# Kernel tuning notes

Hardware: AMD Instinct MI355X
Metric: run time of the kernel (lower is better)

The kernel has to match this reference:

```python
import jax, jax.numpy as jnp
import numpy as np

N = 100000   # nodes
E = 1250000  # edges
D = 64       # in = hidden = out channels
LN_EPS = 1e-5
L2_EPS = 1e-12


def setup_inputs() -> dict:
    key = jax.random.key(0)
    ks = jax.random.split(key, 16)
    s = 1.0 / np.sqrt(D)
    inp = {
        "x": jax.random.normal(ks[0], (N, D), jnp.float32),
        "edge_index": jax.random.randint(ks[1], (2, E), 0, N, dtype=jnp.int64),
    }
    for i in range(3):  # SAGEConv i: out = mean_aggr @ Wl + bl + x @ Wr
        inp[f"Wl{i}"] = jax.random.normal(ks[2 + 2 * i], (D, D), jnp.float32) * s
        inp[f"bl{i}"] = jnp.zeros((D,), jnp.float32)
        inp[f"Wr{i}"] = jax.random.normal(ks[3 + 2 * i], (D, D), jnp.float32) * s
    for i in range(2):  # LayerNorm after layers 0,1
        inp[f"g{i}"] = jnp.ones((D,), jnp.float32)
        inp[f"b{i}"] = jnp.zeros((D,), jnp.float32)
    return inp


def _sage_conv(x, src, dst, Wl, bl, Wr):
    # PyG SAGEConv(aggr='mean'): lin_l(mean of neighbor msgs) + lin_r(x)
    agg = jax.ops.segment_sum(x[src], dst, num_segments=N)          # [N, D]
    deg = jax.ops.segment_sum(jnp.ones((src.shape[0],), x.dtype), dst, num_segments=N)
    mean = agg / jnp.maximum(deg, 1.0)[:, None]
    return mean @ Wl + bl + x @ Wr


def _layer_norm(h, g, b):
    mu = jnp.mean(h, axis=-1, keepdims=True)
    var = jnp.mean((h - mu) ** 2, axis=-1, keepdims=True)
    return (h - mu) * jax.lax.rsqrt(var + LN_EPS) * g + b


def reference(x, edge_index, Wl0, bl0, Wr0, Wl1, bl1, Wr1, Wl2, bl2, Wr2, g0, b0, g1, b1):
    src, dst = edge_index[0], edge_index[1]
    Ws = [(Wl0, bl0, Wr0), (Wl1, bl1, Wr1), (Wl2, bl2, Wr2)]
    lns = [(g0, b0), (g1, b1)]
    h = x
    for i in range(3):
        res = h  # residual projections are Identity (equal dims)
        h = _sage_conv(h, src, dst, *Ws[i])
        if i < 2:
            h = _layer_norm(h, *lns[i])
            h = jax.nn.relu(h)
            h = h + res
            # dropout is identity in eval mode
        else:
            h = h + res
    # F.normalize(p=2, dim=1)
    nrm = jnp.sqrt(jnp.sum(h * h, axis=1, keepdims=True))
    return h / jnp.maximum(nrm, L2_EPS)
```

## Files before the change

kernel.cpp:

```cpp
#include <hip/hip_runtime.h>

#define DD   64
#define WSTR 136
#define SSTR 72
#define BSH  9
#define BNODES 512
#define BCAPSH 13

typedef unsigned int uint32;
typedef __attribute__((ext_vector_type(8))) short short8;
typedef __attribute__((ext_vector_type(4))) float f32x4;

__device__ __forceinline__ unsigned short f2bf_rne(float f) {
    uint32 u = __float_as_uint(f);
    u += 0x7fffu + ((u >> 16) & 1u);
    return (unsigned short)(u >> 16);
}
__device__ __forceinline__ float bf_lo(uint32 w) { return __uint_as_float(w << 16); }
__device__ __forceinline__ float bf_hi(uint32 w) { return __uint_as_float(w & 0xffff0000u); }
__device__ __forceinline__ float bf2f(unsigned short s) {
    return __uint_as_float(((uint32)s) << 16);
}

__global__ __launch_bounds__(256) void cvt_kernel(const float* __restrict__ x,
                                                  unsigned short* __restrict__ xb,
                                                  int n4, int* __restrict__ gCnt) {
    if (blockIdx.x == 0 && threadIdx.x < 256) gCnt[threadIdx.x] = 0;
    int i = blockIdx.x * 256 + threadIdx.x;
    if (i < n4) {
        float4 v = ((const float4*)x)[i];
        ushort4 p;
        p.x = f2bf_rne(v.x); p.y = f2bf_rne(v.y);
        p.z = f2bf_rne(v.z); p.w = f2bf_rne(v.w);
        ((ushort4*)xb)[i] = p;
    }
}

__global__ __launch_bounds__(1024) void bucket_kernel(const int* __restrict__ src,
                                                      const int* __restrict__ dst,
                                                      int* __restrict__ gCnt,
                                                      int2* __restrict__ buf, int E) {
    __shared__ int ldsCnt[256];
    __shared__ int base[256];
    const int t = threadIdx.x;
    if (t < 256) ldsCnt[t] = 0;
    __syncthreads();

    const int e0 = blockIdx.x * 4096;
    int bk[4], rk[4], sv[4], dv[4];
#pragma unroll
    for (int k = 0; k < 4; ++k) {
        int e = e0 + k * 1024 + t;
        bk[k] = -1;
        if (e < E) {
            dv[k] = dst[e];
            sv[k] = src[e];
            bk[k] = dv[k] >> BSH;
            rk[k] = atomicAdd(&ldsCnt[bk[k]], 1);
        }
    }
    __syncthreads();
    if (t < 256 && ldsCnt[t] > 0) base[t] = atomicAdd(&gCnt[t], ldsCnt[t]);
    __syncthreads();
#pragma unroll
    for (int k = 0; k < 4; ++k) {
        if (bk[k] >= 0) {
            int pos = (bk[k] << BCAPSH) + base[bk[k]] + rk[k];
            buf[pos] = make_int2(sv[k], dv[k]);
        }
    }
}

__global__ __launch_bounds__(512) void csr_build(const int2* __restrict__ buf,
                                                 const int* __restrict__ gCnt,
                                                 int* __restrict__ offsets,
                                                 int* __restrict__ csr, int N, int E) {
    __shared__ int c1[BNODES];
    __shared__ int s[BNODES];
    __shared__ int sg2[256];
    const int b = blockIdx.x;
    const int t = threadIdx.x;
    if (t < 256) sg2[t] = gCnt[t];
    c1[t] = 0;
    __syncthreads();
    for (int d = 1; d < 256; d <<= 1) {
        int v = (t < 256 && t >= d) ? sg2[t - d] : 0;
        __syncthreads();
        if (t < 256 && t >= d) sg2[t] += v;
        __syncthreads();
    }
    const int base = (b == 0) ? 0 : sg2[b - 1];
    const int cnt = gCnt[b];
    const int2* bb = buf + ((size_t)b << BCAPSH);
    for (int i = t; i < cnt; i += 512) atomicAdd(&c1[bb[i].y & (BNODES - 1)], 1);
    __syncthreads();

    int v = c1[t];
    s[t] = v;
    __syncthreads();
    for (int d = 1; d < BNODES; d <<= 1) {
        int u = (t >= d) ? s[t - d] : 0;
        __syncthreads();
        if (t >= d) s[t] += u;
        __syncthreads();
    }
    int excl = s[t] - v;
    const int node = (b << BSH) + t;
    if (node < N) offsets[node] = base + excl;
    if (b == 0 && t == 0) offsets[N] = E;
    __syncthreads();
    s[t] = excl;
    c1[t] = 0;
    __syncthreads();

    for (int i = t; i < cnt; i += 512) {
        int2 e = bb[i];
        int d = e.y & (BNODES - 1);
        int r = atomicAdd(&c1[d], 1);
        csr[base + s[d] + r] = e.x;
    }
}

template <int MODE>
__global__ __launch_bounds__(256, 4) void sage_layer(
    const unsigned short* __restrict__ hbin,
    const int* __restrict__ offsets,
    const int* __restrict__ csr,
    const float* __restrict__ Wl,
    const float* __restrict__ bl,
    const float* __restrict__ Wr,
    const float* __restrict__ g,
    const float* __restrict__ bta,
    unsigned short* __restrict__ hbout,
    float* __restrict__ out,
    int N) {
    __shared__ unsigned short sWt[64 * WSTR];
    __shared__ unsigned short sSelf[64 * SSTR];
    __shared__ unsigned short sMean[64 * SSTR];
    __shared__ float sbl[DD], sg[DD], sb[DD];

    const int t = threadIdx.x;
    const int nbase = blockIdx.x * 64;

    for (int idx = t; idx < 2 * DD * DD; idx += 256) {
        int k = idx >> 6, c = idx & 63;
        float v = (k < DD) ? Wl[idx] : Wr[idx - DD * DD];
        sWt[c * WSTR + k] = f2bf_rne(v);
    }
    if (t < DD) {
        sbl[t] = bl[t];
        if (MODE == 0) { sg[t] = g[t]; sb[t] = bta[t]; }
    }

#pragma unroll
    for (int r = 0; r < 2; ++r) {
        int idx = r * 256 + t;
        int row = idx >> 3;
        int qq  = idx & 7;
        int n   = min(nbase + row, N - 1);
        uint4 v = ((const uint4*)(hbin + (size_t)n * DD))[qq];
        *(uint4*)(&sSelf[row * SSTR + qq * 8]) = v;
    }

    {
        const int grp = t >> 3;
        const int q   = t & 7;
#pragma unroll 1
        for (int rep = 0; rep < 2; ++rep) {
            int local = grp + rep * 32;
            int node  = nbase + local;
            float a0 = 0.f, a1 = 0.f, a2 = 0.f, a3 = 0.f,
                  a4 = 0.f, a5 = 0.f, a6 = 0.f, a7 = 0.f;
            int deg = 0;
            if (node < N) {
                int off0 = offsets[node];
                int off1 = offsets[node + 1];
                deg = off1 - off0;
                for (int j = off0; j < off1; j += 8) {
                    uint4 v[8];
#pragma unroll
                    for (int s = 0; s < 8; ++s) {
                        uint4 tt = make_uint4(0u, 0u, 0u, 0u);
                        int idx = j + s;
                        if (idx < off1) {
                            int sn = __builtin_nontemporal_load(&csr[idx]);
                            tt = ((const uint4*)(hbin + (size_t)sn * DD))[q];
                        }
                        v[s] = tt;
                    }
#pragma unroll
                    for (int s = 0; s < 8; ++s) {
                        a0 += bf_lo(v[s].x); a1 += bf_hi(v[s].x);
                        a2 += bf_lo(v[s].y); a3 += bf_hi(v[s].y);
                        a4 += bf_lo(v[s].z); a5 += bf_hi(v[s].z);
                        a6 += bf_lo(v[s].w); a7 += bf_hi(v[s].w);
                    }
                }
            }
            float invd = 1.0f / fmaxf((float)deg, 1.0f);
            ushort4 pa, pb;
            pa.x = f2bf_rne(a0 * invd); pa.y = f2bf_rne(a1 * invd);
            pa.z = f2bf_rne(a2 * invd); pa.w = f2bf_rne(a3 * invd);
            pb.x = f2bf_rne(a4 * invd); pb.y = f2bf_rne(a5 * invd);
            pb.z = f2bf_rne(a6 * invd); pb.w = f2bf_rne(a7 * invd);
            *(ushort4*)(&sMean[local * SSTR + q * 8])     = pa;
            *(ushort4*)(&sMean[local * SSTR + q * 8 + 4]) = pb;
        }
    }
    __syncthreads();

    const int wave = t >> 6;
    const int lane = t & 63;
    const int quad = lane >> 4;
    const int n16  = lane & 15;
    const int lbase = wave * 16;

    short8 af[4];
    af[0] = *(const short8*)(&sMean[(lbase + n16) * SSTR + quad * 8]);
    af[1] = *(const short8*)(&sMean[(lbase + n16) * SSTR + 32 + quad * 8]);
    af[2] = *(const short8*)(&sSelf[(lbase + n16) * SSTR + quad * 8]);
    af[3] = *(const short8*)(&sSelf[(lbase + n16) * SSTR + 32 + quad * 8]);

    f32x4 acc[4];
#pragma unroll
    for (int j = 0; j < 4; ++j) {
        float bv = sbl[j * 16 + n16];
        acc[j] = (f32x4){bv, bv, bv, bv};
    }
#pragma unroll
    for (int s = 0; s < 4; ++s) {
#pragma unroll
        for (int j = 0; j < 4; ++j) {
            short8 bf = *(const short8*)(&sWt[(j * 16 + n16) * WSTR + s * 32 + quad * 8]);
            acc[j] = __builtin_amdgcn_mfma_f32_16x16x32_bf16(af[s], bf, acc[j], 0, 0, 0);
        }
    }

#pragma unroll
    for (int i = 0; i < 4; ++i) {
        const int lrow = lbase + quad * 4 + i;
        const int rr   = nbase + lrow;
        float res[4];
#pragma unroll
        for (int j = 0; j < 4; ++j)
            res[j] = bf2f(sSelf[lrow * SSTR + j * 16 + n16]);
        float o[4];
        if (MODE == 0) {
            float s4 = acc[0][i] + acc[1][i] + acc[2][i] + acc[3][i];
            s4 += __shfl_xor(s4, 1, 64);
            s4 += __shfl_xor(s4, 2, 64);
            s4 += __shfl_xor(s4, 4, 64);
            s4 += __shfl_xor(s4, 8, 64);
            float mu = s4 * (1.0f / 64.0f);
            float d0 = acc[0][i] - mu, d1 = acc[1][i] - mu,
                  d2 = acc[2][i] - mu, d3 = acc[3][i] - mu;
            float qq = d0 * d0 + d1 * d1 + d2 * d2 + d3 * d3;
            qq += __shfl_xor(qq, 1, 64);
            qq += __shfl_xor(qq, 2, 64);
            qq += __shfl_xor(qq, 4, 64);
            qq += __shfl_xor(qq, 8, 64);
            float rstd = rsqrtf(qq * (1.0f / 64.0f) + 1e-5f);
            o[0] = fmaxf(d0 * rstd * sg[ 0 + n16] + sb[ 0 + n16], 0.f) + res[0];
            o[1] = fmaxf(d1 * rstd * sg[16 + n16] + sb[16 + n16], 0.f) + res[1];
            o[2] = fmaxf(d2 * rstd * sg[32 + n16] + sb[32 + n16], 0.f) + res[2];
            o[3] = fmaxf(d3 * rstd * sg[48 + n16] + sb[48 + n16], 0.f) + res[3];
        } else {
            o[0] = acc[0][i] + res[0];
            o[1] = acc[1][i] + res[1];
            o[2] = acc[2][i] + res[2];
            o[3] = acc[3][i] + res[3];
            float qq = o[0] * o[0] + o[1] * o[1] + o[2] * o[2] + o[3] * o[3];
            qq += __shfl_xor(qq, 1, 64);
            qq += __shfl_xor(qq, 2, 64);
            qq += __shfl_xor(qq, 4, 64);
            qq += __shfl_xor(qq, 8, 64);
            float inv = 1.0f / fmaxf(sqrtf(qq), 1e-12f);
            o[0] *= inv; o[1] *= inv; o[2] *= inv; o[3] *= inv;
        }
        if (rr < N) {
#pragma unroll
            for (int j = 0; j < 4; ++j) {
                if (MODE == 0)
                    hbout[(size_t)rr * DD + j * 16 + n16] = f2bf_rne(o[j]);
                else
                    out[(size_t)rr * DD + j * 16 + n16] = o[j];
            }
        }
    }
}

extern "C" void kernel_launch(void* const* d_in, const int* in_sizes, int n_in,
                              void* d_out, int out_size, void* d_ws, size_t ws_size,
                              hipStream_t stream) {
    const float* x   = (const float*)d_in[0];
    const int*   ei  = (const int*)d_in[1];
    const float* Wl0 = (const float*)d_in[2];
    const float* bl0 = (const float*)d_in[3];
    const float* Wr0 = (const float*)d_in[4];
    const float* Wl1 = (const float*)d_in[5];
    const float* bl1 = (const float*)d_in[6];
    const float* Wr1 = (const float*)d_in[7];
    const float* Wl2 = (const float*)d_in[8];
    const float* bl2 = (const float*)d_in[9];
    const float* Wr2 = (const float*)d_in[10];
    const float* g0  = (const float*)d_in[11];
    const float* b0  = (const float*)d_in[12];
    const float* g1  = (const float*)d_in[13];
    const float* b1  = (const float*)d_in[14];

    const int N = in_sizes[0] / DD;
    const int E = in_sizes[1] / 2;
    const int* src = ei;
    const int* dst = ei + E;
    const int NB = (N + BNODES - 1) >> BSH;

    int2* bucketBuf = (int2*)d_ws;
    unsigned short* HB0 = (unsigned short*)(bucketBuf + ((size_t)256 << BCAPSH));
    unsigned short* HB1 = HB0 + (size_t)N * DD;
    int*   csr     = (int*)(HB1 + (size_t)N * DD);
    int*   offsets = csr + E;
    int*   gCnt    = offsets + (N + 1);
    float* out     = (float*)d_out;

    const int tiles = (N + 63) / 64;
    const int n4    = N * DD / 4;
    const int cgrid = (n4 + 255) / 256;
    const int bgrid = (E + 4095) / 4096;

    cvt_kernel<<<cgrid, 256, 0, stream>>>(x, HB0, n4, gCnt);
    bucket_kernel<<<bgrid, 1024, 0, stream>>>(src, dst, gCnt, bucketBuf, E);
    csr_build<<<NB, 512, 0, stream>>>(bucketBuf, gCnt, offsets, csr, N, E);

    sage_layer<0><<<tiles, 256, 0, stream>>>(HB0, offsets, csr, Wl0, bl0, Wr0,
                                             g0, b0, HB1, nullptr, N);
    sage_layer<0><<<tiles, 256, 0, stream>>>(HB1, offsets, csr, Wl1, bl1, Wr1,
                                             g1, b1, HB0, nullptr, N);
    sage_layer<1><<<tiles, 256, 0, stream>>>(HB0, offsets, csr, Wl2, bl2, Wr2,
                                             nullptr, nullptr, nullptr, out, N);
}
```

Baseline: 313.6 us.

## Pre-convert weights once to global bf16, read MFMA operands from global, use wave-shuffle scans

Weight transposition and bf16 conversion for all three layers move into the existing conversion kernel, written once to a global buffer. The SAGE layer kernels then read the B operands straight from global (likely cache-resident) instead of rebuilding a 17KB LDS copy in every block, and the smaller LDS footprint lets the launch bounds request 8 blocks per SM instead of 4. The CSR build also replaces its LDS Hillis-Steele scans with wave shuffle reductions and scans, which cuts the number of barriers. In exchange, the MFMA B fragments become global loads, adding latency in the inner loop.

```diff
diff --git a/kernel.cpp b/kernel.cpp
--- a/kernel.cpp
+++ b/kernel.cpp
@@ -1,7 +1,6 @@
 #include <hip/hip_runtime.h>
 
 #define DD   64
-#define WSTR 136
 #define SSTR 72
 #define BSH  9
 #define BNODES 512
@@ -22,17 +21,32 @@
     return __uint_as_float(((uint32)s) << 16);
 }
 
-__global__ __launch_bounds__(256) void cvt_kernel(const float* __restrict__ x,
-                                                  unsigned short* __restrict__ xb,
-                                                  int n4, int* __restrict__ gCnt) {
-    if (blockIdx.x == 0 && threadIdx.x < 256) gCnt[threadIdx.x] = 0;
-    int i = blockIdx.x * 256 + threadIdx.x;
-    if (i < n4) {
-        float4 v = ((const float4*)x)[i];
+__global__ __launch_bounds__(256) void cvt_kernel(
+    const float* __restrict__ x, unsigned short* __restrict__ xb, int n4,
+    int* __restrict__ gCnt,
+    const float* __restrict__ Wl0, const float* __restrict__ Wr0,
+    const float* __restrict__ Wl1, const float* __restrict__ Wr1,
+    const float* __restrict__ Wl2, const float* __restrict__ Wr2,
+    unsigned short* __restrict__ wtg) {
+    const int gid = blockIdx.x * 256 + threadIdx.x;
+    if (blockIdx.x == 0) gCnt[threadIdx.x] = 0;
+    if (gid < 3 * 2 * DD * DD) {
+        int layer = gid >> 13;
+        int idx   = gid & 8191;
+        int k = idx >> 6, c = idx & 63;
+        const float* Wsrc;
+        if (layer == 0)      Wsrc = (k < DD) ? Wl0 : Wr0;
+        else if (layer == 1) Wsrc = (k < DD) ? Wl1 : Wr1;
+        else                 Wsrc = (k < DD) ? Wl2 : Wr2;
+        float v = Wsrc[(k & (DD - 1)) * DD + c];
+        wtg[layer * 8192 + c * 128 + k] = f2bf_rne(v);
+    }
+    if (gid < n4) {
+        float4 v = ((const float4*)x)[gid];
         ushort4 p;
         p.x = f2bf_rne(v.x); p.y = f2bf_rne(v.y);
         p.z = f2bf_rne(v.z); p.w = f2bf_rne(v.w);
-        ((ushort4*)xb)[i] = p;
+        ((ushort4*)xb)[gid] = p;
     }
 }
 
@@ -76,40 +90,46 @@
                                                  int* __restrict__ offsets,
                                                  int* __restrict__ csr, int N, int E) {
     __shared__ int c1[BNODES];
-    __shared__ int s[BNODES];
-    __shared__ int sg2[256];
+    __shared__ int s2[BNODES];
+    __shared__ int sw[16];
     const int b = blockIdx.x;
     const int t = threadIdx.x;
-    if (t < 256) sg2[t] = gCnt[t];
+    const int lane = t & 63;
+    const int w = t >> 6;
+
+    int gv = (t < 256 && t < b) ? gCnt[t] : 0;
+#pragma unroll
+    for (int d = 1; d < 64; d <<= 1) gv += __shfl_xor(gv, d, 64);
+    if (lane == 0) sw[w] = gv;
     c1[t] = 0;
     __syncthreads();
-    for (int d = 1; d < 256; d <<= 1) {
-        int v = (t < 256 && t >= d) ? sg2[t - d] : 0;
-        __syncthreads();
-        if (t < 256 && t >= d) sg2[t] += v;
-        __syncthreads();
-    }
-    const int base = (b == 0) ? 0 : sg2[b - 1];
+    int base = 0;
+#pragma unroll
+    for (int i = 0; i < 8; ++i) base += sw[i];
+
     const int cnt = gCnt[b];
     const int2* bb = buf + ((size_t)b << BCAPSH);
     for (int i = t; i < cnt; i += 512) atomicAdd(&c1[bb[i].y & (BNODES - 1)], 1);
     __syncthreads();
 
     int v = c1[t];
-    s[t] = v;
-    __syncthreads();
-    for (int d = 1; d < BNODES; d <<= 1) {
-        int u = (t >= d) ? s[t - d] : 0;
-        __syncthreads();
-        if (t >= d) s[t] += u;
-        __syncthreads();
-    }
-    int excl = s[t] - v;
+    int x = v;
+#pragma unroll
+    for (int d = 1; d < 64; d <<= 1) {
+        int y = __shfl_up(x, d, 64);
+        if (lane >= d) x += y;
+    }
+    if (lane == 63) sw[8 + w] = x;
+    __syncthreads();
+    int woff = 0;
+    for (int i = 0; i < w; ++i) woff += sw[8 + i];
+    int excl = x + woff - v;
+
     const int node = (b << BSH) + t;
     if (node < N) offsets[node] = base + excl;
     if (b == 0 && t == 0) offsets[N] = E;
-    __syncthreads();
-    s[t] = excl;
+
+    s2[t] = excl;
     c1[t] = 0;
     __syncthreads();
 
@@ -117,24 +137,22 @@
         int2 e = bb[i];
         int d = e.y & (BNODES - 1);
         int r = atomicAdd(&c1[d], 1);
-        csr[base + s[d] + r] = e.x;
+        csr[base + s2[d] + r] = e.x;
     }
 }
 
 template <int MODE>
-__global__ __launch_bounds__(256, 4) void sage_layer(
+__global__ __launch_bounds__(256, 8) void sage_layer(
     const unsigned short* __restrict__ hbin,
     const int* __restrict__ offsets,
     const int* __restrict__ csr,
-    const float* __restrict__ Wl,
+    const unsigned short* __restrict__ wt,
     const float* __restrict__ bl,
-    const float* __restrict__ Wr,
     const float* __restrict__ g,
     const float* __restrict__ bta,
     unsigned short* __restrict__ hbout,
     float* __restrict__ out,
     int N) {
-    __shared__ unsigned short sWt[64 * WSTR];
     __shared__ unsigned short sSelf[64 * SSTR];
     __shared__ unsigned short sMean[64 * SSTR];
     __shared__ float sbl[DD], sg[DD], sb[DD];
@@ -142,11 +160,6 @@
     const int t = threadIdx.x;
     const int nbase = blockIdx.x * 64;
 
-    for (int idx = t; idx < 2 * DD * DD; idx += 256) {
-        int k = idx >> 6, c = idx & 63;
-        float v = (k < DD) ? Wl[idx] : Wr[idx - DD * DD];
-        sWt[c * WSTR + k] = f2bf_rne(v);
-    }
     if (t < DD) {
         sbl[t] = bl[t];
         if (MODE == 0) { sg[t] = g[t]; sb[t] = bta[t]; }
@@ -231,7 +244,7 @@
     for (int s = 0; s < 4; ++s) {
 #pragma unroll
         for (int j = 0; j < 4; ++j) {
-            short8 bf = *(const short8*)(&sWt[(j * 16 + n16) * WSTR + s * 32 + quad * 8]);
+            short8 bf = *(const short8*)(wt + (j * 16 + n16) * 128 + s * 32 + quad * 8);
             acc[j] = __builtin_amdgcn_mfma_f32_16x16x32_bf16(af[s], bf, acc[j], 0, 0, 0);
         }
     }
@@ -320,6 +333,8 @@
     int*   csr     = (int*)(HB1 + (size_t)N * DD);
     int*   offsets = csr + E;
     int*   gCnt    = offsets + (N + 1);
+    unsigned short* wtg =
+        (unsigned short*)(((size_t)(gCnt + 256) + 15) & ~(size_t)15);
     float* out     = (float*)d_out;
 
     const int tiles = (N + 63) / 64;
@@ -327,14 +342,15 @@
     const int cgrid = (n4 + 255) / 256;
     const int bgrid = (E + 4095) / 4096;
 
-    cvt_kernel<<<cgrid, 256, 0, stream>>>(x, HB0, n4, gCnt);
+    cvt_kernel<<<cgrid, 256, 0, stream>>>(x, HB0, n4, gCnt,
+                                          Wl0, Wr0, Wl1, Wr1, Wl2, Wr2, wtg);
     bucket_kernel<<<bgrid, 1024, 0, stream>>>(src, dst, gCnt, bucketBuf, E);
     csr_build<<<NB, 512, 0, stream>>>(bucketBuf, gCnt, offsets, csr, N, E);
 
-    sage_layer<0><<<tiles, 256, 0, stream>>>(HB0, offsets, csr, Wl0, bl0, Wr0,
-                                             g0, b0, HB1, nullptr, N);
-    sage_layer<0><<<tiles, 256, 0, stream>>>(HB1, offsets, csr, Wl1, bl1, Wr1,
-                                             g1, b1, HB0, nullptr, N);
-    sage_layer<1><<<tiles, 256, 0, stream>>>(HB0, offsets, csr, Wl2, bl2, Wr2,
-                                             nullptr, nullptr, nullptr, out, N);
-}
+    sage_layer<0><<<tiles, 256, 0, stream>>>(HB0, offsets, csr, wtg,
+                                             bl0, g0, b0, HB1, nullptr, N);
+    sage_layer<0><<<tiles, 256, 0, stream>>>(HB1, offsets, csr, wtg + 8192,
+                                             bl1, g1, b1, HB0, nullptr, N);
+    sage_layer<1><<<tiles, 256, 0, stream>>>(HB0, offsets, csr, wtg + 16384,
+                                             bl2, nullptr, nullptr, nullptr, out, N);
+}
```

Result: slower. 447.5 us (+42.7%).
